# Kernel tuning notes

Measured on AMD Instinct MI355X. Metric: run time of the kernel, lower is better.

## Reference

```python
import jax, jax.numpy as jnp
import numpy as np

B, T, I, H, L, O = 8192, 204, 5, 24, 10, 612

def setup_inputs() -> dict:
    key = jax.random.key(0)
    ks = jax.random.split(key, 10)
    s_ih = 1.0 / np.sqrt(H)
    inp = {
        "x": jax.random.normal(ks[0], (B, T, I), dtype=jnp.float32),
        # torch nn.LSTM params: weight_ih_l0 [4H,I], weight_hh_l0 [4H,H], biases [4H]
        "W_ih": jax.random.uniform(ks[1], (4 * H, I), jnp.float32, -s_ih, s_ih),
        "W_hh": jax.random.uniform(ks[2], (4 * H, H), jnp.float32, -s_ih, s_ih),
        "b_ih": jax.random.uniform(ks[3], (4 * H,), jnp.float32, -s_ih, s_ih),
        "b_hh": jax.random.uniform(ks[4], (4 * H,), jnp.float32, -s_ih, s_ih),
        "fc0_w": jax.random.uniform(ks[5], (L, H * T), jnp.float32, -1 / np.sqrt(H * T), 1 / np.sqrt(H * T)),
        "fc0_b": jax.random.uniform(ks[6], (L,), jnp.float32, -1 / np.sqrt(H * T), 1 / np.sqrt(H * T)),
        "out_w": jax.random.uniform(ks[7], (O, L), jnp.float32, -1 / np.sqrt(L), 1 / np.sqrt(L)),
        "out_b": jax.random.uniform(ks[8], (O,), jnp.float32, -1 / np.sqrt(L), 1 / np.sqrt(L)),
    }
    return inp

def _lstm_forward(x, W_ih, W_hh, b_ih, b_hh):
    # Precompute input projections for all timesteps: [B,T,4H] -> time-major [T,B,4H]
    x_proj = jnp.einsum("bti,gi->btg", x, W_ih) + b_ih
    x_proj = jnp.swapaxes(x_proj, 0, 1)
    h0 = jnp.zeros((x.shape[0], W_hh.shape[1]), x.dtype)
    c0 = jnp.zeros_like(h0)

    def step(carry, xt):
        h, c = carry
        gates = xt + h @ W_hh.T + b_hh  # [B,4H]; torch gate order i,f,g,o
        i, f, g, o = jnp.split(gates, 4, axis=-1)
        c = jax.nn.sigmoid(f) * c + jax.nn.sigmoid(i) * jnp.tanh(g)
        h = jax.nn.sigmoid(o) * jnp.tanh(c)
        return (h, c), h

    _, hs = jax.lax.scan(step, (h0, c0), x_proj)  # hs: [T,B,H]
    return jnp.swapaxes(hs, 0, 1)  # [B,T,H]

def reference(x, W_ih, W_hh, b_ih, b_hh, fc0_w, fc0_b, out_w, out_b):
    h = _lstm_forward(x, W_ih, W_hh, b_ih, b_hh)       # [B,T,H]
    h = h.reshape(h.shape[0], -1)                       # [B, T*H]
    h = jax.nn.relu(h @ fc0_w.T + fc0_b)                # [B, L]
    return h @ out_w.T + out_b                          # [B, O]
```

## Files before the change

kernel.cpp:

```cpp
#include <hip/hip_runtime.h>
#include <math.h>

#define T_  204
#define I_  5
#define H_  24
#define L_  10
#define O_  612
#define Bsz 8192

typedef _Float16 half8 __attribute__((ext_vector_type(8)));
typedef _Float16 half2t __attribute__((ext_vector_type(2)));
typedef float    float4t __attribute__((ext_vector_type(4)));

union U16B { float4t f4; half8 h8; float f[4]; _Float16 h[8]; half2t h2[4]; };

__device__ __forceinline__ float fast_rcp(float x){ return __builtin_amdgcn_rcpf(x); }
__device__ __forceinline__ float fast_ex2(float x){ return __builtin_amdgcn_exp2f(x); }
__device__ __forceinline__ half2t pk2(float a, float b){
    return __builtin_bit_cast(half2t, __builtin_amdgcn_cvt_pkrtz(a, b));
}

#define MFMA16(a,b,c) __builtin_amdgcn_mfma_f32_16x16x32_f16((a),(b),(c),0,0,0)

#define L2E  1.44269504f
#define L2E2 2.88539008f

__device__ __forceinline__ int unit_of(int q, int T) {
    return (q < 3) ? (8*q + T) : (8*(T >> 1) + 6 + (T & 1));
}

__global__ __launch_bounds__(64)
void pack_fc0(const float* __restrict__ fc0_w, float4t* __restrict__ dst)
{
    const int t = blockIdx.x, lane = threadIdx.x;
    const int m = lane & 15, q = lane >> 4;
    U16B v;
    #pragma unroll
    for (int i = 0; i < 8; ++i) {
        const int k = 8*q + i;
        float f = (m < L_ && k < H_) ? fc0_w[m*(T_*H_) + t*H_ + k] : 0.0f;
        v.h[i] = (_Float16)f;
    }
    dst[t*64 + lane] = v.f4;
}

#define ACT1(Dv, cc, hh)                                                        \
  {                                                                             \
    const float ei = fast_ex2((Dv)[0] * -L2E);                                  \
    const float ef = fast_ex2((Dv)[1] * -L2E);                                  \
    const float eg = fast_ex2((Dv)[2] *  L2E2);                                 \
    const float eo = fast_ex2((Dv)[3] * -L2E);                                  \
    const float Dn1 = 1.f + ef;                                                 \
    const float Dn2 = 1.f + ei;                                                 \
    const float Dn3 = eg + 1.f;                                                 \
    const float G   = eg - 1.f;                                                 \
    const float P   = Dn2 * Dn3;                                                \
    const float R1  = fast_rcp(Dn1 * P);                                        \
    const float nm  = fmaf((cc), P, Dn1 * G);                                   \
    (cc) = nm * R1;                                                             \
    const float es  = fast_ex2(__builtin_fabsf(cc) * -L2E2);                    \
    const float R2  = fast_rcp((1.f + eo) * (1.f + es));                        \
    (hh) = __builtin_copysignf((1.f - es) * R2, (cc));                          \
  }

#define POS(K, faK, xsK)                                                        \
  {                                                                             \
    float4t D0 = MFMA16(Ag[0], B.h8, zf4);                                      \
    float4t D1 = MFMA16(Ag[1], B.h8, zf4);                                      \
    float4t D2 = MFMA16(Ag[2], B.h8, zf4);                                      \
    float4t D3 = MFMA16(Ag[3], B.h8, zf4);                                      \
    float4t D4 = MFMA16(Ag[4], B.h8, zf4);                                      \
    float4t D5 = MFMA16(Ag[5], B.h8, zf4);                                      \
    float hh0, hh1, hh2, hh3, hh4, hh5;                                         \
    ACT1(D0, c0, hh0)                                                           \
    ACT1(D1, c1, hh1)                                                           \
    ACT1(D2, c2, hh2)                                                           \
    ACT1(D3, c3, hh3)                                                           \
    ACT1(D4, c4, hh4)                                                           \
    ACT1(D5, c5, hh5)                                                           \
    const float P0 = __builtin_bit_cast(float, pk2(hh0, hh1));                  \
    const float P1 = __builtin_bit_cast(float, pk2(hh2, hh3));                  \
    const float P2 = __builtin_bit_cast(float, pk2(hh4, hh5));                  \
    const float r0 = __shfl(P0, src, 64);                                       \
    const float r1 = __shfl(P1, src, 64);                                       \
    const float r2 = __shfl(P2, src, 64);                                       \
    const float rcv = (q == 0) ? r0 : ((q == 1) ? r1 : r2);                     \
    if (q < 3) {                                                                \
      B.h2[0] = __builtin_bit_cast(half2t, P0);                                 \
      B.h2[1] = __builtin_bit_cast(half2t, P1);                                 \
      B.h2[2] = __builtin_bit_cast(half2t, P2);                                 \
      B.h2[3] = __builtin_bit_cast(half2t, rcv);                                \
    } else {                                                                    \
      B.h2[0] = pk2(xsK[0], xsK[1]);                                            \
      B.h2[1] = pk2(xsK[2], xsK[3]);                                            \
      B.h2[2] = pk2(xsK[4], 1.0f);                                              \
      B.h2[3] = pk2(0.f, 0.f);                                                  \
    }                                                                           \
    { U16B fF; fF.f4 = faK;                                                     \
      accF = MFMA16(fF.h8, B.h8, accF); }                                       \
          \
    { const int tf = (t + K + 4 < T_) ? t + K + 4 : T_ - 1;                     \
      faK = fc0A[tf*64 + lane]; }                                               \
    if (q == 3) {                                                               \
      const int txi = (t + K + 5 < T_) ? t + K + 5 : T_ - 1;                    \
      const float* xq = xp + txi*I_;                                            \
      _Pragma("unroll")                                                         \
      for (int i = 0; i < I_; ++i) xsK[i] = xq[i];                              \
    }                                                                           \
  }

__global__ __launch_bounds__(64)
void lstm_mfma(const float* __restrict__ x,
               const float* __restrict__ W_ih,
               const float* __restrict__ W_hh,
               const float* __restrict__ b_ih,
               const float* __restrict__ b_hh,
               const float* __restrict__ fc0_b,
               const float* __restrict__ out_w,
               const float* __restrict__ out_b,
               const float4t* __restrict__ fc0A,
               float* __restrict__ out)
{
    __shared__ __align__(16) _Float16 actL[16*24];

    const int lane = threadIdx.x;
    const int m = lane & 15;
    const int q = lane >> 4;
    const int elem = blockIdx.x * 16 + m;
    const int src = 48 + m;

    const float4t zf4 = {0.f, 0.f, 0.f, 0.f};

    half8 Ag[6];
    #pragma unroll
    for (int T6 = 0; T6 < 6; ++T6) {
        const int u = unit_of(m >> 2, T6);
        const int srow = (m & 3) * H_ + u;
        float wv[8];
        if (q < 3) {
            const float4t* pw = (const float4t*)(W_hh + srow*H_ + 8*q);
            float4t wa = pw[0], wb = pw[1];
            #pragma unroll
            for (int i = 0; i < 4; ++i) { wv[i] = wa[i]; wv[4+i] = wb[i]; }
        } else {
            #pragma unroll
            for (int i = 0; i < 8; ++i) wv[i] = 0.f;
            #pragma unroll
            for (int i = 0; i < I_; ++i) wv[i] = W_ih[srow*I_ + i];
            wv[5] = b_ih[srow] + b_hh[srow];
        }
        U16B tw;
        #pragma unroll
        for (int i = 0; i < 8; ++i) tw.h[i] = (_Float16)wv[i];
        Ag[T6] = tw.h8;
    }

    const float* xp = x + (size_t)elem * (T_*I_);

    U16B B;
    if (q == 3) {
        B.h2[0] = pk2(xp[0], xp[1]);
        B.h2[1] = pk2(xp[2], xp[3]);
        B.h2[2] = pk2(xp[4], 1.0f);
        B.h2[3] = pk2(0.f, 0.f);
    } else {
        B.f4 = zf4;
    }

    float4t fa0 = fc0A[0*64 + lane];
    float4t fa1 = fc0A[1*64 + lane];
    float4t fa2 = fc0A[2*64 + lane];
    float4t fa3 = fc0A[3*64 + lane];
    float xs0[I_] = {0,0,0,0,0}, xs1[I_] = {0,0,0,0,0};
    float xs2[I_] = {0,0,0,0,0}, xs3[I_] = {0,0,0,0,0};
    if (q == 3) {
        #pragma unroll
        for (int i = 0; i < I_; ++i) {
            xs0[i] = xp[1*I_ + i];
            xs1[i] = xp[2*I_ + i];
            xs2[i] = xp[3*I_ + i];
            xs3[i] = xp[4*I_ + i];
        }
    }

    float c0 = 0.f, c1 = 0.f, c2 = 0.f, c3 = 0.f, c4 = 0.f, c5 = 0.f;
    float4t accF = zf4;

    #pragma unroll 1
    for (int t = 0; t < T_; t += 4) {
        POS(0, fa0, xs0)
        POS(1, fa1, xs1)
        POS(2, fa2, xs2)
        POS(3, fa3, xs3)
    }

    float av[4];
    #pragma unroll
    for (int r = 0; r < 4; ++r) {
        const int l = 4*q + r;
        const float fb = (l < L_) ? fc0_b[l] : 0.f;
        const float v = accF[r] + fb;
        av[r] = (l < L_) ? fmaxf(v, 0.f) : 0.f;
    }
    *(half2t*)(&actL[m*24 + 4*q])     = pk2(av[0], av[1]);
    *(half2t*)(&actL[m*24 + 4*q + 2]) = pk2(av[2], av[3]);
    __builtin_amdgcn_wave_barrier();

    U16B Ba;
    if (q < 2) Ba.f4 = *(const float4t*)(&actL[m*24 + q*8]);
    else       Ba.f4 = zf4;

    for (int Tt = 0; Tt < 39; ++Tt) {
        const int row = 16*Tt + m;
        float w0=0.f,w1=0.f,w2=0.f,w3=0.f,w4=0.f,w5=0.f,w6=0.f,w7=0.f;
        if (row < O_ && q < 2) {
            const float2* p2 = (const float2*)(out_w + row*L_);
            if (q == 0) {
                float2 a = p2[0], b = p2[1], cc = p2[2], dd = p2[3];
                w0=a.x; w1=a.y; w2=b.x; w3=b.y; w4=cc.x; w5=cc.y; w6=dd.x; w7=dd.y;
            } else {
                float2 a = p2[4];
                w0=a.x; w1=a.y;
            }
        }
        U16B Aw;
        Aw.h2[0] = pk2(w0,w1); Aw.h2[1] = pk2(w2,w3);
        Aw.h2[2] = pk2(w4,w5); Aw.h2[3] = pk2(w6,w7);

        float4t dd = MFMA16(Aw.h8, Ba.h8, zf4);

        const int ob = 16*Tt + 4*q;
        if (ob < O_) {
            const float4t bias = *(const float4t*)(out_b + ob);
            #pragma unroll
            for (int r = 0; r < 4; ++r) dd[r] += bias[r];
            *(float4t*)(out + (size_t)elem*O_ + ob) = dd;
        }
    }
}

extern "C" void kernel_launch(void* const* d_in, const int* in_sizes, int n_in,
                              void* d_out, int out_size, void* d_ws, size_t ws_size,
                              hipStream_t stream)
{
    const float* x     = (const float*)d_in[0];
    const float* W_ih  = (const float*)d_in[1];
    const float* W_hh  = (const float*)d_in[2];
    const float* b_ih  = (const float*)d_in[3];
    const float* b_hh  = (const float*)d_in[4];
    const float* fc0_w = (const float*)d_in[5];
    const float* fc0_b = (const float*)d_in[6];
    const float* out_w = (const float*)d_in[7];
    const float* out_b = (const float*)d_in[8];
    float* out = (float*)d_out;
    (void)ws_size;

    pack_fc0<<<dim3(T_), dim3(64), 0, stream>>>(fc0_w, (float4t*)d_ws);
    lstm_mfma<<<dim3(Bsz/16), dim3(64), 0, stream>>>(
        x, W_ih, W_hh, b_ih, b_hh, fc0_b, out_w, out_b,
        (const float4t*)d_ws, out);
}
```

Baseline: 214.5 us.

## Split LSTM gate activations across lane halves, eight batch elements per wave

Each wave now handles 8 batch elements instead of 16. The two 8-column halves of the MFMA output split the six gate tiles between them, so each lane evaluates three activation chains per timestep instead of six. Hidden-state fragments are exchanged through extra lane shuffles to rebuild the B operand, and the grid doubles to twice as many blocks. This is meant to shorten the serial per-timestep critical path and raise wave occupancy. The cost is duplicated MFMA work per element and more shuffle traffic per step.

```diff
diff --git a/kernel.cpp b/kernel.cpp
--- a/kernel.cpp
+++ b/kernel.cpp
@@ -71,25 +71,30 @@
     float4t D3 = MFMA16(Ag[3], B.h8, zf4);                                      \
     float4t D4 = MFMA16(Ag[4], B.h8, zf4);                                      \
     float4t D5 = MFMA16(Ag[5], B.h8, zf4);                                      \
-    float hh0, hh1, hh2, hh3, hh4, hh5;                                         \
-    ACT1(D0, c0, hh0)                                                           \
-    ACT1(D1, c1, hh1)                                                           \
-    ACT1(D2, c2, hh2)                                                           \
-    ACT1(D3, c3, hh3)                                                           \
-    ACT1(D4, c4, hh4)                                                           \
-    ACT1(D5, c5, hh5)                                                           \
-    const float P0 = __builtin_bit_cast(float, pk2(hh0, hh1));                  \
-    const float P1 = __builtin_bit_cast(float, pk2(hh2, hh3));                  \
-    const float P2 = __builtin_bit_cast(float, pk2(hh4, hh5));                  \
-    const float r0 = __shfl(P0, src, 64);                                       \
-    const float r1 = __shfl(P1, src, 64);                                       \
-    const float r2 = __shfl(P2, src, 64);                                       \
-    const float rcv = (q == 0) ? r0 : ((q == 1) ? r1 : r2);                     \
+    const float4t E0 = mhi ? D3 : D0;                                           \
+    const float4t E1 = mhi ? D4 : D1;                                           \
+    const float4t E2 = mhi ? D5 : D2;                                           \
+    float h0, h1, h2;                                                           \
+    ACT1(E0, c0, h0)                                                            \
+    ACT1(E1, c1, h1)                                                            \
+    ACT1(E2, c2, h2)                                                            \
+      \
+    const float s0 = __shfl(h0, sPart, 64);                                     \
+    const float s1 = __shfl(h1, sPart, 64);                                     \
+    const float s2 = __shfl(h2, sPart, 64);                                     \
+    const float rA = __shfl(h0, srcA, 64);                                      \
+    const float rB = __shfl(h1, srcB, 64);                                      \
+    const float rC = __shfl(h2, srcC, 64);                                      \
     if (q < 3) {                                                                \
-      B.h2[0] = __builtin_bit_cast(half2t, P0);                                 \
-      B.h2[1] = __builtin_bit_cast(half2t, P1);                                 \
-      B.h2[2] = __builtin_bit_cast(half2t, P2);                                 \
-      B.h2[3] = __builtin_bit_cast(half2t, rcv);                                \
+         \
+      B.h2[0] = pk2(mhi ? s0 : h0, mhi ? s1 : h1);                              \
+      B.h2[1] = pk2(mhi ? s2 : h2, mhi ? h0 : s0);                              \
+      B.h2[2] = pk2(mhi ? h1 : s1, mhi ? h2 : s2);                              \
+       \
+       \
+      const float pa = (q == 0) ? rA : ((q == 1) ? rC : rB);                    \
+      const float pb = (q == 0) ? rB : ((q == 1) ? rA : rC);                    \
+      B.h2[3] = pk2(pa, pb);                                                    \
     } else {                                                                    \
       B.h2[0] = pk2(xsK[0], xsK[1]);                                            \
       B.h2[1] = pk2(xsK[2], xsK[3]);                                            \
@@ -126,8 +131,14 @@
     const int lane = threadIdx.x;
     const int m = lane & 15;
     const int q = lane >> 4;
-    const int elem = blockIdx.x * 16 + m;
-    const int src = 48 + m;
+    const int mb = m & 7;
+    const bool mhi = (m >= 8);
+    const int eb = blockIdx.x * 8 + mb;
+
+    const int sPart = lane ^ 8;
+    const int srcA = ((q == 1) ? 56 : 48) + mb;
+    const int srcB = ((q == 2) ? 56 : 48) + mb;
+    const int srcC = ((q == 2) ? 56 : 48) + mb;
 
     const float4t zf4 = {0.f, 0.f, 0.f, 0.f};
 
@@ -155,7 +166,7 @@
         Ag[T6] = tw.h8;
     }
 
-    const float* xp = x + (size_t)elem * (T_*I_);
+    const float* xp = x + (size_t)eb * (T_*I_);
 
     U16B B;
     if (q == 3) {
@@ -183,7 +194,7 @@
         }
     }
 
-    float c0 = 0.f, c1 = 0.f, c2 = 0.f, c3 = 0.f, c4 = 0.f, c5 = 0.f;
+    float c0 = 0.f, c1 = 0.f, c2 = 0.f;
     float4t accF = zf4;
 
     #pragma unroll 1
@@ -230,11 +241,11 @@
         float4t dd = MFMA16(Aw.h8, Ba.h8, zf4);
 
         const int ob = 16*Tt + 4*q;
-        if (ob < O_) {
+        if (ob < O_ && m < 8) {
             const float4t bias = *(const float4t*)(out_b + ob);
             #pragma unroll
             for (int r = 0; r < 4; ++r) dd[r] += bias[r];
-            *(float4t*)(out + (size_t)elem*O_ + ob) = dd;
+            *(float4t*)(out + (size_t)eb*O_ + ob) = dd;
         }
     }
 }
@@ -256,7 +267,7 @@
     (void)ws_size;
 
     pack_fc0<<<dim3(T_), dim3(64), 0, stream>>>(fc0_w, (float4t*)d_ws);
-    lstm_mfma<<<dim3(Bsz/16), dim3(64), 0, stream>>>(
+    lstm_mfma<<<dim3(Bsz/8), dim3(64), 0, stream>>>(
         x, W_ih, W_hh, b_ih, b_hh, fc0_b, out_w, out_b,
         (const float4t*)d_ws, out);
 }
```

Result: faster. 195.2 us (-9.0%).
